# Kernel tuning notes

Hardware: AMD Instinct MI355X
Metric: run time of the kernel (lower is better)

The kernel has to match this reference:

```python
import jax, jax.numpy as jnp
import numpy as np

D_MODEL = 768
NUM_HEADS = 12
HEAD_DIM = D_MODEL // NUM_HEADS
SEQ = 4096
BATCH = 1


def setup_inputs() -> dict:
    key = jax.random.key(0)
    ks = jax.random.split(key, 6)
    scale = 1.0 / np.sqrt(D_MODEL)
    x = jax.random.normal(ks[0], (BATCH, SEQ, D_MODEL), dtype=jnp.float32)
    mask = jnp.tril(jnp.ones((SEQ, SEQ), dtype=bool))[None, None]  # [1,1,S,S] causal
    Wq = jax.random.normal(ks[1], (D_MODEL, D_MODEL), dtype=jnp.float32) * scale
    Wk = jax.random.normal(ks[2], (D_MODEL, D_MODEL), dtype=jnp.float32) * scale
    Wv = jax.random.normal(ks[3], (D_MODEL, D_MODEL), dtype=jnp.float32) * scale
    Wo = jax.random.normal(ks[4], (D_MODEL, D_MODEL), dtype=jnp.float32) * scale
    bo = jax.random.normal(ks[5], (D_MODEL,), dtype=jnp.float32) * 0.01
    return {"x": x, "mask": mask, "Wq": Wq, "Wk": Wk, "Wv": Wv, "Wo": Wo, "bo": bo}


def _rope_tables(seq_len, head_dim, dtype):
    # inv_freq over even dims; emb = cat(freqs, freqs) but only the first half
    # participates in the well-defined rotation (x1/x2 have head_dim//2 channels)
    inv_freq = 1.0 / (10000.0 ** (jnp.arange(0, head_dim, 2, dtype=dtype) / head_dim))
    t = jnp.arange(seq_len, dtype=dtype)
    freqs = t[:, None] * inv_freq[None, :]  # [S, head_dim//2]
    return jnp.cos(freqs), jnp.sin(freqs)


def _apply_rotary(xh, cos, sin):
    # xh: [B,H,S,hd]; cos/sin: [S, hd//2]
    x1 = xh[..., ::2]
    x2 = xh[..., 1::2]
    # faithful to source: concatenated (not interleaved) rotated halves
    return jnp.concatenate([x1 * cos - x2 * sin, x1 * sin + x2 * cos], axis=-1)


def reference(x, mask, Wq, Wk, Wv, Wo, bo):
    B, S, D = x.shape
    H, hd = NUM_HEADS, HEAD_DIM
    def split_heads(y):
        return y.reshape(B, S, H, hd).transpose(0, 2, 1, 3)  # [B,H,S,hd]
    q = split_heads(x @ Wq.T)
    k = split_heads(x @ Wk.T)
    v = split_heads(x @ Wv.T)
    cos, sin = _rope_tables(S, hd, x.dtype)
    q = _apply_rotary(q, cos, sin)
    k = _apply_rotary(k, cos, sin)
    scores = jnp.einsum('bhqd,bhkd->bhqk', q, k) / jnp.sqrt(jnp.asarray(hd, x.dtype))
    scores = jnp.where(mask, scores, jnp.asarray(-1e9, x.dtype))
    attn = jax.nn.softmax(scores, axis=-1)  # dropout is identity in eval
    out = jnp.einsum('bhqk,bhkd->bhqd', attn, v)
    out = out.transpose(0, 2, 1, 3).reshape(B, S, D)
    return out @ Wo.T + bo
```

## Files before the change

### kernel.cpp

```cpp
#include <hip/hip_runtime.h>
#include <hip/hip_bf16.h>
#include <math.h>

#define SEQ 4096
#define DM  768
#define NH  12
#define HD  64
#define PER ((size_t)NH * SEQ * HD)
#define XN  ((size_t)SEQ * DM)
#define WN  ((size_t)DM * DM)

typedef __attribute__((ext_vector_type(8))) short bf16x8;
typedef __attribute__((ext_vector_type(4))) short s16x4;
typedef __attribute__((ext_vector_type(4))) float f32x4;

#define MFMA(a, b, c) __builtin_amdgcn_mfma_f32_16x16x32_bf16((a), (b), (c), 0, 0, 0)

#if __has_builtin(__builtin_amdgcn_exp2f)
#define EXP2(x) __builtin_amdgcn_exp2f(x)
#else
#define EXP2(x) exp2f(x)
#endif

#define SWZ(row, blk) (((row) << 6) + ((((blk) ^ ((row) & 7))) << 3))

__device__ __forceinline__ unsigned short f2b(float f) {
    unsigned int u = __float_as_uint(f);
    u += 0x7FFFu + ((u >> 16) & 1u);
    return (unsigned short)(u >> 16);
}

__global__ __launch_bounds__(256) void prep_kernel(
    const float* __restrict__ x,  const float* __restrict__ wq,
    const float* __restrict__ wk, const float* __restrict__ wv,
    const float* __restrict__ wo,
    unsigned short* __restrict__ dstbase, float2* __restrict__ rope)
{
    const float* srcs[5] = {x, wq, wk, wv, wo};
    const size_t n4s[5]  = {XN / 4, WN / 4, WN / 4, WN / 4, WN / 4};
    unsigned short* d = dstbase;
    for (int rg = 0; rg < 5; ++rg) {
        const float4* s4 = (const float4*)srcs[rg];
        s16x4* d4 = (s16x4*)d;
        for (size_t i = (size_t)blockIdx.x * 256 + threadIdx.x; i < n4s[rg];
             i += (size_t)gridDim.x * 256) {
            const float4 v = s4[i];
            s16x4 p;
            p.x = (short)f2b(v.x); p.y = (short)f2b(v.y);
            p.z = (short)f2b(v.z); p.w = (short)f2b(v.w);
            d4[i] = p;
        }
        d += n4s[rg] * 4;
    }
    for (int g = blockIdx.x * 256 + threadIdx.x; g < 131072; g += gridDim.x * 256) {
        const int row = g >> 5, fi = g & 31;
        const float invf = expf(-(float)fi * 0.28782313662425576f);
        float sn, cs;
        sincosf((float)row * invf, &sn, &cs);
        rope[row * 32 + fi] = make_float2(cs, sn);
    }
}

__global__ __launch_bounds__(256) void qkv_mfma(
    const float* __restrict__ x,  const unsigned short* __restrict__ xb,
    const float* __restrict__ Wq, const float* __restrict__ Wk, const float* __restrict__ Wv,
    const unsigned short* __restrict__ Wqb, const unsigned short* __restrict__ Wkb,
    const unsigned short* __restrict__ Wvb,
    const float2* __restrict__ rope,
    unsigned short* __restrict__ Qo, unsigned short* __restrict__ Ko,
    unsigned short* __restrict__ Vo, int fast)
{
    __shared__ __align__(16) unsigned short Xs[2][4096];
    __shared__ __align__(16) unsigned short Ws[2][4096];
    __shared__ unsigned short VL[64 * 66];

    const int t    = threadIdx.x;
    const int w    = t >> 6;
    const int lane = t & 63;
    const int quad = lane >> 4;
    const int l16  = lane & 15;

    const int nt_b = blockIdx.y;
    const float* W; const unsigned short* Wb; int region;
    if (nt_b < 12)      { W = Wq; Wb = Wqb; region = 0; }
    else if (nt_b < 24) { W = Wk; Wb = Wkb; region = 1; }
    else                { W = Wv; Wb = Wvb; region = 2; }
    const int h  = nt_b % 12;
    const int s0 = blockIdx.x * 64;
    const int n0 = h * 64;

    f32x4 acc[4] = {{0,0,0,0},{0,0,0,0},{0,0,0,0},{0,0,0,0}};
    const int prow = t >> 3, pblk = t & 7;

    bf16x8 xr0, xr1, wr0, wr1;
    if (fast) {
        xr0 = *(const bf16x8*)&xb[(size_t)(s0 + prow) * DM + pblk * 8];
        xr1 = *(const bf16x8*)&xb[(size_t)(s0 + prow + 32) * DM + pblk * 8];
        wr0 = *(const bf16x8*)&Wb[(size_t)(n0 + prow) * DM + pblk * 8];
        wr1 = *(const bf16x8*)&Wb[(size_t)(n0 + prow + 32) * DM + pblk * 8];
        *(bf16x8*)&Xs[0][SWZ(prow, pblk)]      = xr0;
        *(bf16x8*)&Xs[0][SWZ(prow + 32, pblk)] = xr1;
        *(bf16x8*)&Ws[0][SWZ(prow, pblk)]      = wr0;
        *(bf16x8*)&Ws[0][SWZ(prow + 32, pblk)] = wr1;
    } else {
        for (int e = t; e < 1024; e += 256) {
            const int row = e >> 4, c4 = e & 15;
            const int off = SWZ(row, c4 >> 1) + (c4 & 1) * 4;
            const float4 xv = *(const float4*)&x[(size_t)(s0 + row) * DM + c4 * 4];
            s16x4 px; px.x = (short)f2b(xv.x); px.y = (short)f2b(xv.y);
            px.z = (short)f2b(xv.z); px.w = (short)f2b(xv.w);
            *(s16x4*)&Xs[0][off] = px;
            const float4 wv = *(const float4*)&W[(size_t)(n0 + row) * DM + c4 * 4];
            s16x4 pw; pw.x = (short)f2b(wv.x); pw.y = (short)f2b(wv.y);
            pw.z = (short)f2b(wv.z); pw.w = (short)f2b(wv.w);
            *(s16x4*)&Ws[0][off] = pw;
        }
    }
    __syncthreads();

    for (int kt = 0; kt < 12; ++kt) {
        const unsigned short* Xb  = Xs[kt & 1];
        const unsigned short* Wbt = Ws[kt & 1];
        if (fast && kt < 11) {
            const int k0 = (kt + 1) * 64;
            xr0 = *(const bf16x8*)&xb[(size_t)(s0 + prow) * DM + k0 + pblk * 8];
            xr1 = *(const bf16x8*)&xb[(size_t)(s0 + prow + 32) * DM + k0 + pblk * 8];
            wr0 = *(const bf16x8*)&Wb[(size_t)(n0 + prow) * DM + k0 + pblk * 8];
            wr1 = *(const bf16x8*)&Wb[(size_t)(n0 + prow + 32) * DM + k0 + pblk * 8];
        }
        const bf16x8 a0 = *(const bf16x8*)&Xb[SWZ(16 * w + l16, quad)];
        const bf16x8 a1 = *(const bf16x8*)&Xb[SWZ(16 * w + l16, 4 + quad)];
        #pragma unroll
        for (int nt = 0; nt < 4; ++nt) {
            const bf16x8 b0 = *(const bf16x8*)&Wbt[SWZ(16 * nt + l16, quad)];
            const bf16x8 b1 = *(const bf16x8*)&Wbt[SWZ(16 * nt + l16, 4 + quad)];
            acc[nt] = MFMA(a0, b0, acc[nt]);
            acc[nt] = MFMA(a1, b1, acc[nt]);
        }
        if (kt < 11) {
            const int nb = (kt + 1) & 1;
            if (fast) {
                *(bf16x8*)&Xs[nb][SWZ(prow, pblk)]      = xr0;
                *(bf16x8*)&Xs[nb][SWZ(prow + 32, pblk)] = xr1;
                *(bf16x8*)&Ws[nb][SWZ(prow, pblk)]      = wr0;
                *(bf16x8*)&Ws[nb][SWZ(prow + 32, pblk)] = wr1;
            } else {
                const int k0 = (kt + 1) * 64;
                for (int e = t; e < 1024; e += 256) {
                    const int row = e >> 4, c4 = e & 15;
                    const int off = SWZ(row, c4 >> 1) + (c4 & 1) * 4;
                    const float4 xv = *(const float4*)&x[(size_t)(s0 + row) * DM + k0 + c4 * 4];
                    s16x4 px; px.x = (short)f2b(xv.x); px.y = (short)f2b(xv.y);
                    px.z = (short)f2b(xv.z); px.w = (short)f2b(xv.w);
                    *(s16x4*)&Xs[nb][off] = px;
                    const float4 wv = *(const float4*)&W[(size_t)(n0 + row) * DM + k0 + c4 * 4];
                    s16x4 pw; pw.x = (short)f2b(wv.x); pw.y = (short)f2b(wv.y);
                    pw.z = (short)f2b(wv.z); pw.w = (short)f2b(wv.w);
                    *(s16x4*)&Ws[nb][off] = pw;
                }
            }
        }
        __syncthreads();
    }

    const size_t headoff = (size_t)h * SEQ * HD;
    if (region <= 1) {
        unsigned short* dst = (region == 0) ? Qo : Ko;
        const float qsc = (region == 0) ? 0.18033688011112042f : 1.0f;
        #pragma unroll
        for (int nt = 0; nt < 4; ++nt)
            #pragma unroll
            for (int r = 0; r < 4; ++r) {
                const int srow = s0 + 16 * w + quad * 4 + r;
                const int d  = nt * 16 + l16;
                const int fi = d >> 1;
                const float own = acc[nt][r] * qsc;
                const float oth = __shfl_xor(own, 1);
                float cs, sn;
                if (fast) {
                    const float2 t2 = rope[srow * 32 + fi];
                    cs = t2.x; sn = t2.y;
                } else {
                    const float invf = expf(-(float)fi * 0.28782313662425576f);
                    sincosf((float)srow * invf, &sn, &cs);
                }
                const float val = (d & 1) ? (oth * sn + own * cs)
                                          : (own * cs - oth * sn);
                dst[headoff + (size_t)srow * HD + ((d & 1) ? 32 : 0) + fi] = f2b(val);
            }
    } else {
        #pragma unroll
        for (int nt = 0; nt < 4; ++nt)
            #pragma unroll
            for (int r = 0; r < 4; ++r)
                VL[(nt * 16 + l16) * 66 + 16 * w + quad * 4 + r] = f2b(acc[nt][r]);
        __syncthreads();
        for (int e = t; e < 2048; e += 256) {
            const int d = e >> 5, sp = e & 31;
            const unsigned int v = (unsigned int)VL[d * 66 + 2 * sp] |
                                   ((unsigned int)VL[d * 66 + 2 * sp + 1] << 16);
            *(unsigned int*)&Vo[headoff + (size_t)d * SEQ + s0 + 2 * sp] = v;
        }
    }
}

__global__ __launch_bounds__(256, 2) void attn_mfma(
    const unsigned short* __restrict__ Q,
    const unsigned short* __restrict__ K,
    const unsigned short* __restrict__ V,
    unsigned short* __restrict__ O,
    float* __restrict__ Part)
{
    __shared__ __align__(16) unsigned char SM[53248];
    unsigned short* Kst = (unsigned short*)SM;
    unsigned short* Vt  = (unsigned short*)(SM + 16384);
    unsigned short* Ps  = (unsigned short*)(SM + 32768);
    float* ACC  = (float*)SM;
    float* ACC2 = (float*)(SM + 32768);
    float* Lx   = (float*)(SM + 51200);

    const int h  = blockIdx.y;
    const int xx = blockIdx.x;
    int i, kstart, nch, domask, partial, pslice;
    if (gridDim.x == 96) {
        if (xx < 64) {
            i = 63 - xx; kstart = 0;
            const int full = ((i * 64 + 63) >> 7) + 1;
            nch = full < 16 ? full : 16;
            domask  = (i <= 31);
            partial = (i >= 32); pslice = 0;
        } else {
            i = 127 - xx; kstart = 2048;
            nch = ((i * 64 + 63 - 2048) >> 7) + 1;
            domask = 1; partial = 1; pslice = 1;
        }
    } else {
        i = 63 - xx; kstart = 0;
        nch = ((i * 64 + 63) >> 7) + 1;
        domask = 1; partial = 0; pslice = 0;
    }
    const int q0 = i * 64;

    const int t    = threadIdx.x;
    const int w    = t >> 6;
    const int lane = t & 63;
    const int quad = lane >> 4;
    const int l16  = lane & 15;
    const size_t headoff = (size_t)h * SEQ * HD;

    for (int e = t; e < 512; e += 256) {
        const int row = e >> 3, bp = e & 7, blk = bp ^ (row & 7);
        *(bf16x8*)&Kst[row * 64 + bp * 8] =
            *(const bf16x8*)&Q[headoff + (size_t)(q0 + row) * HD + blk * 8];
    }
    __syncthreads();
    bf16x8 aQ[4][2];
    #pragma unroll
    for (int qt = 0; qt < 4; ++qt)
        #pragma unroll
        for (int hh = 0; hh < 2; ++hh)
            aQ[qt][hh] = *(const bf16x8*)&Kst[SWZ(16 * qt + l16, 4 * hh + quad)];
    __syncthreads();

    bf16x8 kreg[4], vreg[4];
    #pragma unroll
    for (int ii = 0; ii < 4; ++ii) {
        const int e = t + ii * 256, row = e >> 3, bp = e & 7, blk = bp ^ (row & 7);
        kreg[ii] = *(const bf16x8*)&K[headoff + (size_t)(kstart + row) * HD + blk * 8];
    }
    #pragma unroll
    for (int ii = 0; ii < 4; ++ii) {
        const int e = t + ii * 256, row = e >> 4, bp = e & 15, blk = bp ^ (row & 15);
        vreg[ii] = *(const bf16x8*)&V[headoff + (size_t)row * SEQ + kstart + blk * 8];
    }
    #pragma unroll
    for (int ii = 0; ii < 4; ++ii) {
        const int e = t + ii * 256, row = e >> 3, bp = e & 7;
        *(bf16x8*)&Kst[row * 64 + bp * 8] = kreg[ii];
    }
    #pragma unroll
    for (int ii = 0; ii < 4; ++ii) {
        const int e = t + ii * 256, row = e >> 4, bp = e & 15;
        *(bf16x8*)&Vt[row * 128 + bp * 8] = vreg[ii];
    }
    __syncthreads();

    bf16x8 ones;
    #pragma unroll
    for (int ii = 0; ii < 8; ++ii) ones[ii] = (short)0x3F80;

    f32x4 oT[4][4];
    #pragma unroll
    for (int dt = 0; dt < 4; ++dt)
        #pragma unroll
        for (int qt = 0; qt < 4; ++qt) oT[dt][qt] = (f32x4){0,0,0,0};
    f32x4 lT[4] = {{0,0,0,0},{0,0,0,0},{0,0,0,0},{0,0,0,0}};

    unsigned short* usp = Ps + w * 2560;

    for (int c = 0; c < nch; ++c) {
        const int k0 = kstart + c * 128;

        f32x4 sC[4][2];
        #pragma unroll
        for (int qt = 0; qt < 4; ++qt)
            #pragma unroll
            for (int kt = 0; kt < 2; ++kt) sC[qt][kt] = (f32x4){0,0,0,0};
        #pragma unroll
        for (int kt = 0; kt < 2; ++kt) {
            const int krow = 32 * w + 16 * kt + l16;
            #pragma unroll
            for (int hh = 0; hh < 2; ++hh) {
                const bf16x8 bK = *(const bf16x8*)&Kst[SWZ(krow, 4 * hh + quad)];
                #pragma unroll
                for (int qt = 0; qt < 4; ++qt)
                    sC[qt][kt] = MFMA(aQ[qt][hh], bK, sC[qt][kt]);
            }
        }

        if (c < nch - 1) {
            const int kn = k0 + 128;
            #pragma unroll
            for (int ii = 0; ii < 4; ++ii) {
                const int e = t + ii * 256, row = e >> 3, bp = e & 7, blk = bp ^ (row & 7);
                kreg[ii] = *(const bf16x8*)&K[headoff + (size_t)(kn + row) * HD + blk * 8];
            }
            #pragma unroll
            for (int ii = 0; ii < 4; ++ii) {
                const int e = t + ii * 256, row = e >> 4, bp = e & 15, blk = bp ^ (row & 15);
                vreg[ii] = *(const bf16x8*)&V[headoff + (size_t)row * SEQ + kn + blk * 8];
            }
        }

        if (domask && c == nch - 1) {
            #pragma unroll
            for (int kt = 0; kt < 2; ++kt) {
                const int key = k0 + 32 * w + 16 * kt + l16;
                #pragma unroll
                for (int qt = 0; qt < 4; ++qt)
                    #pragma unroll
                    for (int r = 0; r < 4; ++r)
                        if (key > q0 + 16 * qt + 4 * quad + r) sC[qt][kt][r] = -1e30f;
            }
        }

        #pragma unroll
        for (int qt = 0; qt < 4; ++qt)
            #pragma unroll
            for (int kt = 0; kt < 2; ++kt)
                #pragma unroll
                for (int r = 0; r < 4; ++r)
                    usp[(16 * qt + 4 * quad + r) * 40 + 16 * kt + l16] =
                        f2b(EXP2(sC[qt][kt][r]));
        asm volatile("s_waitcnt lgkmcnt(0)" ::: "memory");

        bf16x8 aV[4];
        #pragma unroll
        for (int dt = 0; dt < 4; ++dt) {
            const int row = 16 * dt + l16;
            aV[dt] = *(const bf16x8*)&Vt[row * 128 + (((4 * w + quad) ^ (row & 15)) << 3)];
        }
        #pragma unroll
        for (int qt = 0; qt < 4; ++qt) {
            const bf16x8 bP = *(const bf16x8*)&usp[(16 * qt + l16) * 40 + quad * 8];
            lT[qt] = MFMA(ones, bP, lT[qt]);
            #pragma unroll
            for (int dt = 0; dt < 4; ++dt)
                oT[dt][qt] = MFMA(aV[dt], bP, oT[dt][qt]);
        }

        __syncthreads();
        if (c < nch - 1) {
            #pragma unroll
            for (int ii = 0; ii < 4; ++ii) {
                const int e = t + ii * 256, row = e >> 3, bp = e & 7;
                *(bf16x8*)&Kst[row * 64 + bp * 8] = kreg[ii];
            }
            #pragma unroll
            for (int ii = 0; ii < 4; ++ii) {
                const int e = t + ii * 256, row = e >> 4, bp = e & 15;
                *(bf16x8*)&Vt[row * 128 + bp * 8] = vreg[ii];
            }
        }
        __syncthreads();
    }

    if (w != 0 && quad == 0) {
        #pragma unroll
        for (int qt = 0; qt < 4; ++qt)
            Lx[w * 64 + 16 * qt + l16] = lT[qt][0];
    }
    if (w == 1) {
        #pragma unroll
        for (int dt = 0; dt < 4; ++dt)
            #pragma unroll
            for (int qt = 0; qt < 4; ++qt)
                *(f32x4*)&ACC[(16 * qt + l16) * 72 + 16 * dt + 4 * quad] = oT[dt][qt];
    }
    __syncthreads();
    if (w == 0) {
        #pragma unroll
        for (int dt = 0; dt < 4; ++dt)
            #pragma unroll
            for (int qt = 0; qt < 4; ++qt)
                oT[dt][qt] += *(const f32x4*)&ACC[(16 * qt + l16) * 72 + 16 * dt + 4 * quad];
    }
    if (w == 2) {
        #pragma unroll
        for (int dt = 0; dt < 4; ++dt)
            #pragma unroll
            for (int qt = 0; qt < 4; ++qt)
                *(f32x4*)&ACC2[(16 * qt + l16) * 72 + 16 * dt + 4 * quad] = oT[dt][qt];
    }
    __syncthreads();
    if (w == 0) {
        #pragma unroll
        for (int dt = 0; dt < 4; ++dt)
            #pragma unroll
            for (int qt = 0; qt < 4; ++qt)
                oT[dt][qt] += *(const f32x4*)&ACC2[(16 * qt + l16) * 72 + 16 * dt + 4 * quad];
    }
    if (w == 3) {
        #pragma unroll
        for (int dt = 0; dt < 4; ++dt)
            #pragma unroll
            for (int qt = 0; qt < 4; ++qt)
                *(f32x4*)&ACC[(16 * qt + l16) * 72 + 16 * dt + 4 * quad] = oT[dt][qt];
    }
    __syncthreads();
    if (w == 0) {
        float ls[4];
        #pragma unroll
        for (int qt = 0; qt < 4; ++qt) {
            #pragma unroll
            for (int dt = 0; dt < 4; ++dt)
                oT[dt][qt] += *(const f32x4*)&ACC[(16 * qt + l16) * 72 + 16 * dt + 4 * quad];
            ls[qt] = lT[qt][0] + Lx[64 + 16 * qt + l16] +
                     Lx[128 + 16 * qt + l16] + Lx[192 + 16 * qt + l16];
        }
        if (!partial) {
            #pragma unroll
            for (int qt = 0; qt < 4; ++qt) {
                const float inv = 1.0f / ls[qt];
                const size_t rowoff = (size_t)(q0 + 16 * qt + l16) * DM + h * HD;
                #pragma unroll
                for (int dt = 0; dt < 4; ++dt) {
                    ushort4 u;
                    u.x = f2b(oT[dt][qt][0] * inv);
                    u.y = f2b(oT[dt][qt][1] * inv);
                    u.z = f2b(oT[dt][qt][2] * inv);
                    u.w = f2b(oT[dt][qt][3] * inv);
                    *(ushort4*)&O[rowoff + 16 * dt + 4 * quad] = u;
                }
            }
        } else {
            float* P = Part + (size_t)(((i - 32) * 12 + h) * 2 + pslice) * 4160;
            #pragma unroll
            for (int dt = 0; dt < 4; ++dt)
                #pragma unroll
                for (int qt = 0; qt < 4; ++qt)
                    *(f32x4*)&P[(16 * qt + l16) * 64 + 16 * dt + 4 * quad] = oT[dt][qt];
            if (quad == 0) {
                #pragma unroll
                for (int qt = 0; qt < 4; ++qt)
                    P[4096 + 16 * qt + l16] = ls[qt];
            }
        }
    }
}

__global__ __launch_bounds__(256) void reduce_attn(
    const float* __restrict__ Part, unsigned short* __restrict__ O)
{
    const int b  = blockIdx.x;
    const int i  = 32 + b / 12, h = b % 12;
    const int q0 = i * 64;
    const float* P0 = Part + (size_t)(b * 2 + 0) * 4160;
    const float* P1 = Part + (size_t)(b * 2 + 1) * 4160;
    __shared__ float linv[64];
    const int t = threadIdx.x;
    if (t < 64) linv[t] = 1.0f / (P0[4096 + t] + P1[4096 + t]);
    __syncthreads();
    for (int idx = t; idx < 4096; idx += 256) {
        const int q = idx >> 6, d = idx & 63;
        const float v = (P0[q * 64 + d] + P1[q * 64 + d]) * linv[q];
        O[(size_t)(q0 + q) * DM + h * HD + d] = f2b(v);
    }
}

__global__ __launch_bounds__(256) void proj_mfma(
    const unsigned short* __restrict__ A,
    const float* __restrict__ Wo, const unsigned short* __restrict__ Wob,
    const float* __restrict__ bo,
    float* __restrict__ out, int fast)
{
    __shared__ __align__(16) unsigned short Xs[2][4096];
    __shared__ __align__(16) unsigned short Ws[2][4096];

    const int t    = threadIdx.x;
    const int w    = t >> 6;
    const int lane = t & 63;
    const int quad = lane >> 4;
    const int l16  = lane & 15;
    const int s0 = blockIdx.x * 64;
    const int n0 = blockIdx.y * 64;
    const int prow = t >> 3, pblk = t & 7;

    f32x4 acc[4] = {{0,0,0,0},{0,0,0,0},{0,0,0,0},{0,0,0,0}};

    bf16x8 ar0, ar1, wr0, wr1;
    ar0 = *(const bf16x8*)&A[(size_t)(s0 + prow) * DM + pblk * 8];
    ar1 = *(const bf16x8*)&A[(size_t)(s0 + prow + 32) * DM + pblk * 8];
    *(bf16x8*)&Xs[0][SWZ(prow, pblk)]      = ar0;
    *(bf16x8*)&Xs[0][SWZ(prow + 32, pblk)] = ar1;
    if (fast) {
        wr0 = *(const bf16x8*)&Wob[(size_t)(n0 + prow) * DM + pblk * 8];
        wr1 = *(const bf16x8*)&Wob[(size_t)(n0 + prow + 32) * DM + pblk * 8];
        *(bf16x8*)&Ws[0][SWZ(prow, pblk)]      = wr0;
        *(bf16x8*)&Ws[0][SWZ(prow + 32, pblk)] = wr1;
    } else {
        for (int e = t; e < 1024; e += 256) {
            const int row = e >> 4, c4 = e & 15;
            const float4 wv = *(const float4*)&Wo[(size_t)(n0 + row) * DM + c4 * 4];
            s16x4 pw; pw.x = (short)f2b(wv.x); pw.y = (short)f2b(wv.y);
            pw.z = (short)f2b(wv.z); pw.w = (short)f2b(wv.w);
            *(s16x4*)&Ws[0][SWZ(row, c4 >> 1) + (c4 & 1) * 4] = pw;
        }
    }
    __syncthreads();

    for (int kt = 0; kt < 12; ++kt) {
        const unsigned short* Xb  = Xs[kt & 1];
        const unsigned short* Wbt = Ws[kt & 1];
        if (kt < 11) {
            const int k0 = (kt + 1) * 64;
            ar0 = *(const bf16x8*)&A[(size_t)(s0 + prow) * DM + k0 + pblk * 8];
            ar1 = *(const bf16x8*)&A[(size_t)(s0 + prow + 32) * DM + k0 + pblk * 8];
            if (fast) {
                wr0 = *(const bf16x8*)&Wob[(size_t)(n0 + prow) * DM + k0 + pblk * 8];
                wr1 = *(const bf16x8*)&Wob[(size_t)(n0 + prow + 32) * DM + k0 + pblk * 8];
            }
        }
        const bf16x8 a0 = *(const bf16x8*)&Xb[SWZ(16 * w + l16, quad)];
        const bf16x8 a1 = *(const bf16x8*)&Xb[SWZ(16 * w + l16, 4 + quad)];
        #pragma unroll
        for (int nt = 0; nt < 4; ++nt) {
            const bf16x8 b0 = *(const bf16x8*)&Wbt[SWZ(16 * nt + l16, quad)];
            const bf16x8 b1 = *(const bf16x8*)&Wbt[SWZ(16 * nt + l16, 4 + quad)];
            acc[nt] = MFMA(a0, b0, acc[nt]);
            acc[nt] = MFMA(a1, b1, acc[nt]);
        }
        if (kt < 11) {
            const int nb = (kt + 1) & 1;
            *(bf16x8*)&Xs[nb][SWZ(prow, pblk)]      = ar0;
            *(bf16x8*)&Xs[nb][SWZ(prow + 32, pblk)] = ar1;
            if (fast) {
                *(bf16x8*)&Ws[nb][SWZ(prow, pblk)]      = wr0;
                *(bf16x8*)&Ws[nb][SWZ(prow + 32, pblk)] = wr1;
            } else {
                const int k0 = (kt + 1) * 64;
                for (int e = t; e < 1024; e += 256) {
                    const int row = e >> 4, c4 = e & 15;
                    const float4 wv = *(const float4*)&Wo[(size_t)(n0 + row) * DM + k0 + c4 * 4];
                    s16x4 pw; pw.x = (short)f2b(wv.x); pw.y = (short)f2b(wv.y);
                    pw.z = (short)f2b(wv.z); pw.w = (short)f2b(wv.w);
                    *(s16x4*)&Ws[nb][SWZ(row, c4 >> 1) + (c4 & 1) * 4] = pw;
                }
            }
        }
        __syncthreads();
    }

    #pragma unroll
    for (int nt = 0; nt < 4; ++nt)
        #pragma unroll
        for (int r = 0; r < 4; ++r) {
            const int srow = s0 + 16 * w + quad * 4 + r;
            const int n    = n0 + nt * 16 + l16;
            out[(size_t)srow * DM + n] = acc[nt][r] + bo[n];
        }
}

extern "C" void kernel_launch(void* const* d_in, const int* in_sizes, int n_in,
                              void* d_out, int out_size, void* d_ws, size_t ws_size,
                              hipStream_t stream) {
    const float* x  = (const float*)d_in[0];
    const float* Wq = (const float*)d_in[2];
    const float* Wk = (const float*)d_in[3];
    const float* Wv = (const float*)d_in[4];
    const float* Wo = (const float*)d_in[5];
    const float* bo = (const float*)d_in[6];
    float* out = (float*)d_out;

    unsigned short* U  = (unsigned short*)d_ws;
    unsigned short* Qw = U;
    unsigned short* Kw = U + PER;
    unsigned short* Vw = U + 2 * PER;
    unsigned short* Ow = U + 3 * PER;
    unsigned short* xb  = U + 4 * PER;
    unsigned short* Wqb = xb + XN;
    unsigned short* Wkb = Wqb + WN;
    unsigned short* Wvb = Wkb + WN;
    unsigned short* Wob = Wvb + WN;
    float2* rope = (float2*)(Wob + WN);
    float*  part = (float*)(rope + 4096 * 32);
    const size_t need  = (char*)part - (char*)d_ws;
    const size_t need2 = need + (size_t)384 * 2 * 4160 * 4;
    const int fast  = (ws_size >= need)  ? 1 : 0;
    const int split = (ws_size >= need2) ? 1 : 0;

    if (fast)
        prep_kernel<<<1024, 256, 0, stream>>>(x, Wq, Wk, Wv, Wo, xb, rope);
    qkv_mfma<<<dim3(SEQ / 64, 36), 256, 0, stream>>>(
        x, xb, Wq, Wk, Wv, Wqb, Wkb, Wvb, rope, Qw, Kw, Vw, fast);
    if (split) {
        attn_mfma<<<dim3(96, NH), 256, 0, stream>>>(Qw, Kw, Vw, Ow, part);
        reduce_attn<<<dim3(384), 256, 0, stream>>>(part, Ow);
    } else {
        attn_mfma<<<dim3(64, NH), 256, 0, stream>>>(Qw, Kw, Vw, Ow, part);
    }
    proj_mfma<<<dim3(SEQ / 64, DM / 64), 256, 0, stream>>>(Ow, Wo, Wob, bo, out, fast);
}
```

Before: 243.3 us.

## Load Q/K/V MFMA fragments directly from global memory, drop LDS staging and barriers

The attention kernel no longer stages K and V tiles through shared memory. Each wave loads its own Q, K and V MFMA operand fragments straight from global memory into registers, and prefetches the next K fragments one chunk ahead. This removes the per-chunk LDS writes and both __syncthreads in the loop, and shrinks the shared allocation, which may allow more blocks per CU. In exchange the global loads are smaller and less coalesced, the V loads are not prefetched, and their latency is exposed unless enough waves are resident.

```diff
diff --git a/kernel.cpp b/kernel.cpp
--- a/kernel.cpp
+++ b/kernel.cpp
@@ -211,13 +211,11 @@
     unsigned short* __restrict__ O,
     float* __restrict__ Part)
 {
-    __shared__ __align__(16) unsigned char SM[53248];
-    unsigned short* Kst = (unsigned short*)SM;
-    unsigned short* Vt  = (unsigned short*)(SM + 16384);
-    unsigned short* Ps  = (unsigned short*)(SM + 32768);
+    __shared__ __align__(16) unsigned char SM[38912];
+    unsigned short* Ps = (unsigned short*)SM;
     float* ACC  = (float*)SM;
-    float* ACC2 = (float*)(SM + 32768);
-    float* Lx   = (float*)(SM + 51200);
+    float* ACC2 = (float*)(SM + 18432);
+    float* Lx   = (float*)(SM + 36864);
 
     const int h  = blockIdx.y;
     const int xx = blockIdx.x;
@@ -247,43 +245,25 @@
     const int quad = lane >> 4;
     const int l16  = lane & 15;
     const size_t headoff = (size_t)h * SEQ * HD;
-
-    for (int e = t; e < 512; e += 256) {
-        const int row = e >> 3, bp = e & 7, blk = bp ^ (row & 7);
-        *(bf16x8*)&Kst[row * 64 + bp * 8] =
-            *(const bf16x8*)&Q[headoff + (size_t)(q0 + row) * HD + blk * 8];
-    }
-    __syncthreads();
+    const unsigned short* Qh = Q + headoff;
+    const unsigned short* Kh = K + headoff;
+    const unsigned short* Vh = V + headoff;
+
     bf16x8 aQ[4][2];
     #pragma unroll
     for (int qt = 0; qt < 4; ++qt)
         #pragma unroll
         for (int hh = 0; hh < 2; ++hh)
-            aQ[qt][hh] = *(const bf16x8*)&Kst[SWZ(16 * qt + l16, 4 * hh + quad)];
-    __syncthreads();
-
-    bf16x8 kreg[4], vreg[4];
+            aQ[qt][hh] = *(const bf16x8*)&Qh[(size_t)(q0 + 16 * qt + l16) * HD +
+                                             32 * hh + 8 * quad];
+
+    bf16x8 bK[2][2];
     #pragma unroll
-    for (int ii = 0; ii < 4; ++ii) {
-        const int e = t + ii * 256, row = e >> 3, bp = e & 7, blk = bp ^ (row & 7);
-        kreg[ii] = *(const bf16x8*)&K[headoff + (size_t)(kstart + row) * HD + blk * 8];
-    }
-    #pragma unroll
-    for (int ii = 0; ii < 4; ++ii) {
-        const int e = t + ii * 256, row = e >> 4, bp = e & 15, blk = bp ^ (row & 15);
-        vreg[ii] = *(const bf16x8*)&V[headoff + (size_t)row * SEQ + kstart + blk * 8];
-    }
-    #pragma unroll
-    for (int ii = 0; ii < 4; ++ii) {
-        const int e = t + ii * 256, row = e >> 3, bp = e & 7;
-        *(bf16x8*)&Kst[row * 64 + bp * 8] = kreg[ii];
-    }
-    #pragma unroll
-    for (int ii = 0; ii < 4; ++ii) {
-        const int e = t + ii * 256, row = e >> 4, bp = e & 15;
-        *(bf16x8*)&Vt[row * 128 + bp * 8] = vreg[ii];
-    }
-    __syncthreads();
+    for (int kt = 0; kt < 2; ++kt)
+        #pragma unroll
+        for (int hh = 0; hh < 2; ++hh)
+            bK[kt][hh] = *(const bf16x8*)&Kh[(size_t)(kstart + 32 * w + 16 * kt + l16) * HD +
+                                             32 * hh + 8 * quad];
 
     bf16x8 ones;
     #pragma unroll
@@ -300,6 +280,23 @@
 
     for (int c = 0; c < nch; ++c) {
         const int k0 = kstart + c * 128;
+        const int kw = k0 + 32 * w;
+
+        bf16x8 aV[4];
+        #pragma unroll
+        for (int dt = 0; dt < 4; ++dt)
+            aV[dt] = *(const bf16x8*)&Vh[(size_t)(16 * dt + l16) * SEQ + kw + 8 * quad];
+
+        bf16x8 bKn[2][2];
+        if (c + 1 < nch) {
+            const int kn = k0 + 128 + 32 * w;
+            #pragma unroll
+            for (int kt = 0; kt < 2; ++kt)
+                #pragma unroll
+                for (int hh = 0; hh < 2; ++hh)
+                    bKn[kt][hh] = *(const bf16x8*)&Kh[(size_t)(kn + 16 * kt + l16) * HD +
+                                                      32 * hh + 8 * quad];
+        }
 
         f32x4 sC[4][2];
         #pragma unroll
@@ -307,30 +304,12 @@
             #pragma unroll
             for (int kt = 0; kt < 2; ++kt) sC[qt][kt] = (f32x4){0,0,0,0};
         #pragma unroll
-        for (int kt = 0; kt < 2; ++kt) {
-            const int krow = 32 * w + 16 * kt + l16;
-            #pragma unroll
-            for (int hh = 0; hh < 2; ++hh) {
-                const bf16x8 bK = *(const bf16x8*)&Kst[SWZ(krow, 4 * hh + quad)];
+        for (int kt = 0; kt < 2; ++kt)
+            #pragma unroll
+            for (int hh = 0; hh < 2; ++hh)
                 #pragma unroll
                 for (int qt = 0; qt < 4; ++qt)
-                    sC[qt][kt] = MFMA(aQ[qt][hh], bK, sC[qt][kt]);
-            }
-        }
-
-        if (c < nch - 1) {
-            const int kn = k0 + 128;
-            #pragma unroll
-            for (int ii = 0; ii < 4; ++ii) {
-                const int e = t + ii * 256, row = e >> 3, bp = e & 7, blk = bp ^ (row & 7);
-                kreg[ii] = *(const bf16x8*)&K[headoff + (size_t)(kn + row) * HD + blk * 8];
-            }
-            #pragma unroll
-            for (int ii = 0; ii < 4; ++ii) {
-                const int e = t + ii * 256, row = e >> 4, bp = e & 15, blk = bp ^ (row & 15);
-                vreg[ii] = *(const bf16x8*)&V[headoff + (size_t)row * SEQ + kn + blk * 8];
-            }
-        }
+                    sC[qt][kt] = MFMA(aQ[qt][hh], bK[kt][hh], sC[qt][kt]);
 
         if (domask && c == nch - 1) {
             #pragma unroll
@@ -354,12 +333,6 @@
                         f2b(EXP2(sC[qt][kt][r]));
         asm volatile("s_waitcnt lgkmcnt(0)" ::: "memory");
 
-        bf16x8 aV[4];
-        #pragma unroll
-        for (int dt = 0; dt < 4; ++dt) {
-            const int row = 16 * dt + l16;
-            aV[dt] = *(const bf16x8*)&Vt[row * 128 + (((4 * w + quad) ^ (row & 15)) << 3)];
-        }
         #pragma unroll
         for (int qt = 0; qt < 4; ++qt) {
             const bf16x8 bP = *(const bf16x8*)&usp[(16 * qt + l16) * 40 + quad * 8];
@@ -369,21 +342,16 @@
                 oT[dt][qt] = MFMA(aV[dt], bP, oT[dt][qt]);
         }
 
-        __syncthreads();
-        if (c < nch - 1) {
-            #pragma unroll
-            for (int ii = 0; ii < 4; ++ii) {
-                const int e = t + ii * 256, row = e >> 3, bp = e & 7;
-                *(bf16x8*)&Kst[row * 64 + bp * 8] = kreg[ii];
-            }
-            #pragma unroll
-            for (int ii = 0; ii < 4; ++ii) {
-                const int e = t + ii * 256, row = e >> 4, bp = e & 15;
-                *(bf16x8*)&Vt[row * 128 + bp * 8] = vreg[ii];
-            }
-        }
-        __syncthreads();
-    }
+        if (c + 1 < nch) {
+            #pragma unroll
+            for (int kt = 0; kt < 2; ++kt)
+                #pragma unroll
+                for (int hh = 0; hh < 2; ++hh)
+                    bK[kt][hh] = bKn[kt][hh];
+        }
+    }
+
+    __syncthreads();
 
     if (w != 0 && quad == 0) {
         #pragma unroll
```

Measured after the change: 251.5 us. 1.03x slower.

## Fuse Q/K/V projections into one block per head, reusing X fragments

Applied to the files above, without the earlier changes.

The QKV kernel now computes all three projections (Q, K, V) for one head and 64-row tile in a single block instead of launching separate blocks per projection. X fragments are loaded straight from global memory into registers, no longer staged through shared memory, and each one feeds MFMAs against all three weight tiles. This cuts redundant X reads by a factor of three and shrinks the grid from 36×64 to 12×64 blocks. The cost is more accumulator registers, 48 KB of shared memory per block, and fewer blocks, which may lower occupancy and parallelism.

```diff
diff --git a/kernel.cpp b/kernel.cpp
--- a/kernel.cpp
+++ b/kernel.cpp
@@ -61,7 +61,7 @@
     }
 }
 
-__global__ __launch_bounds__(256) void qkv_mfma(
+__global__ __launch_bounds__(256) void qkv_fused(
     const float* __restrict__ x,  const unsigned short* __restrict__ xb,
     const float* __restrict__ Wq, const float* __restrict__ Wk, const float* __restrict__ Wv,
     const unsigned short* __restrict__ Wqb, const unsigned short* __restrict__ Wkb,
@@ -70,103 +70,125 @@
     unsigned short* __restrict__ Qo, unsigned short* __restrict__ Ko,
     unsigned short* __restrict__ Vo, int fast)
 {
-    __shared__ __align__(16) unsigned short Xs[2][4096];
-    __shared__ __align__(16) unsigned short Ws[2][4096];
-    __shared__ unsigned short VL[64 * 66];
+    __shared__ __align__(16) unsigned short WshFlat[2 * 3 * 4096];
 
     const int t    = threadIdx.x;
     const int w    = t >> 6;
     const int lane = t & 63;
     const int quad = lane >> 4;
     const int l16  = lane & 15;
-
-    const int nt_b = blockIdx.y;
-    const float* W; const unsigned short* Wb; int region;
-    if (nt_b < 12)      { W = Wq; Wb = Wqb; region = 0; }
-    else if (nt_b < 24) { W = Wk; Wb = Wkb; region = 1; }
-    else                { W = Wv; Wb = Wvb; region = 2; }
-    const int h  = nt_b % 12;
-    const int s0 = blockIdx.x * 64;
-    const int n0 = h * 64;
-
-    f32x4 acc[4] = {{0,0,0,0},{0,0,0,0},{0,0,0,0},{0,0,0,0}};
+    const int h    = blockIdx.y;
+    const int s0   = blockIdx.x * 64;
+    const int n0   = h * 64;
     const int prow = t >> 3, pblk = t & 7;
-
-    bf16x8 xr0, xr1, wr0, wr1;
+    const size_t arow = (size_t)(s0 + 16 * w + l16);
+
+    const unsigned short* Wb[3] = {Wqb, Wkb, Wvb};
+    const float*          Wf[3] = {Wq, Wk, Wv};
+
+    f32x4 acc[3][4];
+    #pragma unroll
+    for (int rg = 0; rg < 3; ++rg)
+        #pragma unroll
+        for (int nt = 0; nt < 4; ++nt) acc[rg][nt] = (f32x4){0, 0, 0, 0};
+
     if (fast) {
-        xr0 = *(const bf16x8*)&xb[(size_t)(s0 + prow) * DM + pblk * 8];
-        xr1 = *(const bf16x8*)&xb[(size_t)(s0 + prow + 32) * DM + pblk * 8];
-        wr0 = *(const bf16x8*)&Wb[(size_t)(n0 + prow) * DM + pblk * 8];
-        wr1 = *(const bf16x8*)&Wb[(size_t)(n0 + prow + 32) * DM + pblk * 8];
-        *(bf16x8*)&Xs[0][SWZ(prow, pblk)]      = xr0;
-        *(bf16x8*)&Xs[0][SWZ(prow + 32, pblk)] = xr1;
-        *(bf16x8*)&Ws[0][SWZ(prow, pblk)]      = wr0;
-        *(bf16x8*)&Ws[0][SWZ(prow + 32, pblk)] = wr1;
+        #pragma unroll
+        for (int rg = 0; rg < 3; ++rg) {
+            *(bf16x8*)&WshFlat[rg * 4096 + SWZ(prow, pblk)] =
+                *(const bf16x8*)&Wb[rg][(size_t)(n0 + prow) * DM + pblk * 8];
+            *(bf16x8*)&WshFlat[rg * 4096 + SWZ(prow + 32, pblk)] =
+                *(const bf16x8*)&Wb[rg][(size_t)(n0 + prow + 32) * DM + pblk * 8];
+        }
     } else {
-        for (int e = t; e < 1024; e += 256) {
-            const int row = e >> 4, c4 = e & 15;
-            const int off = SWZ(row, c4 >> 1) + (c4 & 1) * 4;
-            const float4 xv = *(const float4*)&x[(size_t)(s0 + row) * DM + c4 * 4];
-            s16x4 px; px.x = (short)f2b(xv.x); px.y = (short)f2b(xv.y);
-            px.z = (short)f2b(xv.z); px.w = (short)f2b(xv.w);
-            *(s16x4*)&Xs[0][off] = px;
-            const float4 wv = *(const float4*)&W[(size_t)(n0 + row) * DM + c4 * 4];
-            s16x4 pw; pw.x = (short)f2b(wv.x); pw.y = (short)f2b(wv.y);
-            pw.z = (short)f2b(wv.z); pw.w = (short)f2b(wv.w);
-            *(s16x4*)&Ws[0][off] = pw;
-        }
+        for (int rg = 0; rg < 3; ++rg)
+            for (int e = t; e < 1024; e += 256) {
+                const int row = e >> 4, c4 = e & 15;
+                const float4 wv4 = *(const float4*)&Wf[rg][(size_t)(n0 + row) * DM + c4 * 4];
+                s16x4 pw; pw.x = (short)f2b(wv4.x); pw.y = (short)f2b(wv4.y);
+                pw.z = (short)f2b(wv4.z); pw.w = (short)f2b(wv4.w);
+                *(s16x4*)&WshFlat[rg * 4096 + SWZ(row, c4 >> 1) + (c4 & 1) * 4] = pw;
+            }
+    }
+
+    bf16x8 aX[2];
+    if (fast) {
+        aX[0] = *(const bf16x8*)&xb[arow * DM + 8 * quad];
+        aX[1] = *(const bf16x8*)&xb[arow * DM + 32 + 8 * quad];
     }
     __syncthreads();
 
     for (int kt = 0; kt < 12; ++kt) {
-        const unsigned short* Xb  = Xs[kt & 1];
-        const unsigned short* Wbt = Ws[kt & 1];
+        bf16x8 wpre[6], aXn[2];
         if (fast && kt < 11) {
-            const int k0 = (kt + 1) * 64;
-            xr0 = *(const bf16x8*)&xb[(size_t)(s0 + prow) * DM + k0 + pblk * 8];
-            xr1 = *(const bf16x8*)&xb[(size_t)(s0 + prow + 32) * DM + k0 + pblk * 8];
-            wr0 = *(const bf16x8*)&Wb[(size_t)(n0 + prow) * DM + k0 + pblk * 8];
-            wr1 = *(const bf16x8*)&Wb[(size_t)(n0 + prow + 32) * DM + k0 + pblk * 8];
-        }
-        const bf16x8 a0 = *(const bf16x8*)&Xb[SWZ(16 * w + l16, quad)];
-        const bf16x8 a1 = *(const bf16x8*)&Xb[SWZ(16 * w + l16, 4 + quad)];
-        #pragma unroll
-        for (int nt = 0; nt < 4; ++nt) {
-            const bf16x8 b0 = *(const bf16x8*)&Wbt[SWZ(16 * nt + l16, quad)];
-            const bf16x8 b1 = *(const bf16x8*)&Wbt[SWZ(16 * nt + l16, 4 + quad)];
-            acc[nt] = MFMA(a0, b0, acc[nt]);
-            acc[nt] = MFMA(a1, b1, acc[nt]);
-        }
+            const int k0n = (kt + 1) * 64;
+            #pragma unroll
+            for (int rg = 0; rg < 3; ++rg) {
+                wpre[2 * rg] =
+                    *(const bf16x8*)&Wb[rg][(size_t)(n0 + prow) * DM + k0n + pblk * 8];
+                wpre[2 * rg + 1] =
+                    *(const bf16x8*)&Wb[rg][(size_t)(n0 + prow + 32) * DM + k0n + pblk * 8];
+            }
+            aXn[0] = *(const bf16x8*)&xb[arow * DM + k0n + 8 * quad];
+            aXn[1] = *(const bf16x8*)&xb[arow * DM + k0n + 32 + 8 * quad];
+        }
+        if (!fast) {
+            #pragma unroll
+            for (int hh = 0; hh < 2; ++hh) {
+                const float* p = &x[arow * DM + kt * 64 + 32 * hh + 8 * quad];
+                const float4 v0 = *(const float4*)p;
+                const float4 v1 = *(const float4*)(p + 4);
+                bf16x8 r;
+                r[0] = (short)f2b(v0.x); r[1] = (short)f2b(v0.y);
+                r[2] = (short)f2b(v0.z); r[3] = (short)f2b(v0.w);
+                r[4] = (short)f2b(v1.x); r[5] = (short)f2b(v1.y);
+                r[6] = (short)f2b(v1.z); r[7] = (short)f2b(v1.w);
+                aX[hh] = r;
+            }
+        }
+
+        const unsigned short* Wc = &WshFlat[(kt & 1) * 3 * 4096];
+        #pragma unroll
+        for (int rg = 0; rg < 3; ++rg)
+            #pragma unroll
+            for (int nt = 0; nt < 4; ++nt) {
+                const bf16x8 b0 = *(const bf16x8*)&Wc[rg * 4096 + SWZ(16 * nt + l16, quad)];
+                const bf16x8 b1 = *(const bf16x8*)&Wc[rg * 4096 + SWZ(16 * nt + l16, 4 + quad)];
+                acc[rg][nt] = MFMA(aX[0], b0, acc[rg][nt]);
+                acc[rg][nt] = MFMA(aX[1], b1, acc[rg][nt]);
+            }
+
         if (kt < 11) {
-            const int nb = (kt + 1) & 1;
+            unsigned short* Wn = &WshFlat[((kt + 1) & 1) * 3 * 4096];
             if (fast) {
-                *(bf16x8*)&Xs[nb][SWZ(prow, pblk)]      = xr0;
-                *(bf16x8*)&Xs[nb][SWZ(prow + 32, pblk)] = xr1;
-                *(bf16x8*)&Ws[nb][SWZ(prow, pblk)]      = wr0;
-                *(bf16x8*)&Ws[nb][SWZ(prow + 32, pblk)] = wr1;
+                #pragma unroll
+                for (int rg = 0; rg < 3; ++rg) {
+                    *(bf16x8*)&Wn[rg * 4096 + SWZ(prow, pblk)]      = wpre[2 * rg];
+                    *(bf16x8*)&Wn[rg * 4096 + SWZ(prow + 32, pblk)] = wpre[2 * rg + 1];
+                }
+                aX[0] = aXn[0]; aX[1] = aXn[1];
             } else {
-                const int k0 = (kt + 1) * 64;
-                for (int e = t; e < 1024; e += 256) {
-                    const int row = e >> 4, c4 = e & 15;
-                    const int off = SWZ(row, c4 >> 1) + (c4 & 1) * 4;
-                    const float4 xv = *(const float4*)&x[(size_t)(s0 + row) * DM + k0 + c4 * 4];
-                    s16x4 px; px.x = (short)f2b(xv.x); px.y = (short)f2b(xv.y);
-                    px.z = (short)f2b(xv.z); px.w = (short)f2b(xv.w);
-                    *(s16x4*)&Xs[nb][off] = px;
-                    const float4 wv = *(const float4*)&W[(size_t)(n0 + row) * DM + k0 + c4 * 4];
-                    s16x4 pw; pw.x = (short)f2b(wv.x); pw.y = (short)f2b(wv.y);
-                    pw.z = (short)f2b(wv.z); pw.w = (short)f2b(wv.w);
-                    *(s16x4*)&Ws[nb][off] = pw;
-                }
+                const int k0n = (kt + 1) * 64;
+                for (int rg = 0; rg < 3; ++rg)
+                    for (int e = t; e < 1024; e += 256) {
+                        const int row = e >> 4, c4 = e & 15;
+                        const float4 wv4 =
+                            *(const float4*)&Wf[rg][(size_t)(n0 + row) * DM + k0n + c4 * 4];
+                        s16x4 pw; pw.x = (short)f2b(wv4.x); pw.y = (short)f2b(wv4.y);
+                        pw.z = (short)f2b(wv4.z); pw.w = (short)f2b(wv4.w);
+                        *(s16x4*)&Wn[rg * 4096 + SWZ(row, c4 >> 1) + (c4 & 1) * 4] = pw;
+                    }
             }
         }
         __syncthreads();
     }
 
     const size_t headoff = (size_t)h * SEQ * HD;
-    if (region <= 1) {
-        unsigned short* dst = (region == 0) ? Qo : Ko;
-        const float qsc = (region == 0) ? 0.18033688011112042f : 1.0f;
+
+    #pragma unroll
+    for (int rg = 0; rg < 2; ++rg) {
+        unsigned short* dst = (rg == 0) ? Qo : Ko;
+        const float qsc = (rg == 0) ? 0.18033688011112042f : 1.0f;
         #pragma unroll
         for (int nt = 0; nt < 4; ++nt)
             #pragma unroll
@@ -174,7 +196,7 @@
                 const int srow = s0 + 16 * w + quad * 4 + r;
                 const int d  = nt * 16 + l16;
                 const int fi = d >> 1;
-                const float own = acc[nt][r] * qsc;
+                const float own = acc[rg][nt][r] * qsc;
                 const float oth = __shfl_xor(own, 1);
                 float cs, sn;
                 if (fast) {
@@ -188,19 +210,20 @@
                                           : (own * cs - oth * sn);
                 dst[headoff + (size_t)srow * HD + ((d & 1) ? 32 : 0) + fi] = f2b(val);
             }
-    } else {
-        #pragma unroll
-        for (int nt = 0; nt < 4; ++nt)
-            #pragma unroll
-            for (int r = 0; r < 4; ++r)
-                VL[(nt * 16 + l16) * 66 + 16 * w + quad * 4 + r] = f2b(acc[nt][r]);
-        __syncthreads();
-        for (int e = t; e < 2048; e += 256) {
-            const int d = e >> 5, sp = e & 31;
-            const unsigned int v = (unsigned int)VL[d * 66 + 2 * sp] |
-                                   ((unsigned int)VL[d * 66 + 2 * sp + 1] << 16);
-            *(unsigned int*)&Vo[headoff + (size_t)d * SEQ + s0 + 2 * sp] = v;
-        }
+    }
+
+    unsigned short* VL = WshFlat;
+    #pragma unroll
+    for (int nt = 0; nt < 4; ++nt)
+        #pragma unroll
+        for (int r = 0; r < 4; ++r)
+            VL[(nt * 16 + l16) * 66 + 16 * w + quad * 4 + r] = f2b(acc[2][nt][r]);
+    __syncthreads();
+    for (int e = t; e < 2048; e += 256) {
+        const int d = e >> 5, sp = e & 31;
+        const unsigned int v = (unsigned int)VL[d * 66 + 2 * sp] |
+                               ((unsigned int)VL[d * 66 + 2 * sp + 1] << 16);
+        *(unsigned int*)&Vo[headoff + (size_t)d * SEQ + s0 + 2 * sp] = v;
     }
 }
 
@@ -611,7 +634,7 @@
 
     if (fast)
         prep_kernel<<<1024, 256, 0, stream>>>(x, Wq, Wk, Wv, Wo, xb, rope);
-    qkv_mfma<<<dim3(SEQ / 64, 36), 256, 0, stream>>>(
+    qkv_fused<<<dim3(SEQ / 64, NH), 256, 0, stream>>>(
         x, xb, Wq, Wk, Wv, Wqb, Wkb, Wvb, rope, Qw, Kw, Vw, fast);
     if (split) {
         attn_mfma<<<dim3(96, NH), 256, 0, stream>>>(Qw, Kw, Vw, Ow, part);
```

After: 256.3 us. +5.3%, slower.
